# Kernel optimization log

Hardware: AMD Instinct MI355X
Metric: run time of the kernel (lower is better)

The kernel has to match this reference:

```python
import jax, jax.numpy as jnp
import numpy as np


def _conv1x1(x, w, b):
    # x: [B,C,H,W], w: [O,C], b: [O] -> [B,O,H,W]
    return jnp.einsum('bchw,oc->bohw', x, w) + b[None, :, None, None]


def setup_inputs() -> dict:
    key = jax.random.key(0)
    ks = jax.random.split(key, 11)
    B, C, Ci, H, W = 4, 256, 128, 64, 64
    s_in = 1.0 / np.sqrt(C)
    s_ci = 1.0 / np.sqrt(Ci)
    return {
        'x': jax.random.normal(ks[0], (B, C, H, W), jnp.float32),
        'g_w': jax.random.normal(ks[1], (Ci, C), jnp.float32) * s_in,
        'g_b': jax.random.normal(ks[2], (Ci,), jnp.float32) * 0.01,
        'theta_w': jax.random.normal(ks[3], (Ci, C), jnp.float32) * s_in,
        'theta_b': jax.random.normal(ks[4], (Ci,), jnp.float32) * 0.01,
        'phi_w': jax.random.normal(ks[5], (Ci, C), jnp.float32) * s_in,
        'phi_b': jax.random.normal(ks[6], (Ci,), jnp.float32) * 0.01,
        'wz_w': jax.random.normal(ks[7], (C, Ci), jnp.float32) * s_ci,
        'wz_b': jax.random.normal(ks[8], (C,), jnp.float32) * 0.01,
        'bn_gamma': jax.random.uniform(ks[9], (C,), jnp.float32, 0.5, 1.5),
        'bn_beta': jax.random.normal(ks[10], (C,), jnp.float32) * 0.01,
    }


def reference(x, g_w, g_b, theta_w, theta_b, phi_w, phi_b, wz_w, wz_b, bn_gamma, bn_beta):
    B, C, H, W = x.shape
    Ci = g_w.shape[0]
    N = H * W
    # 1x1 conv projections, flattened over spatial positions
    g_x = _conv1x1(x, g_w, g_b).reshape(B, Ci, N).transpose(0, 2, 1)       # [B,N,Ci]
    theta_x = _conv1x1(x, theta_w, theta_b).reshape(B, Ci, N)              # [B,Ci,N]
    phi_x = _conv1x1(x, phi_w, phi_b).reshape(B, Ci, N)                    # [B,Ci,N]
    # f[b, i, j] = theta_i . phi_j  -> [B,N,N]
    f = jnp.einsum('bci,bcj->bij', theta_x, phi_x)
    # NOTE: softmax over dim=1 (query axis) — faithful to original (non-standard)
    f_div_C = jax.nn.softmax(f, axis=1)
    y = jnp.einsum('bij,bjc->bic', f_div_C, g_x)                           # [B,N,Ci]
    y = y.transpose(0, 2, 1).reshape(B, Ci, H, W)                          # [B,Ci,H,W]
    # W_z: 1x1 conv + BatchNorm2d (training-mode batch statistics)
    w_y = _conv1x1(y, wz_w, wz_b)                                          # [B,C,H,W]
    mean = jnp.mean(w_y, axis=(0, 2, 3), keepdims=True)
    var = jnp.var(w_y, axis=(0, 2, 3), keepdims=True)
    w_y = (w_y - mean) * jax.lax.rsqrt(var + 1e-5)
    w_y = w_y * bn_gamma[None, :, None, None] + bn_beta[None, :, None, None]
    return w_y + x
```

## Files before the change

kernel.cpp:

```cpp
#include <hip/hip_runtime.h>


#define B_  4
#define C_  256
#define CI  128
#define N_  4096
#define NB  (B_*N_)
#define ISPLIT 16
#define MB_ (1u<<20)

typedef _Float16 f16;
typedef f16   f16x8 __attribute__((ext_vector_type(8)));
typedef f16   f16x4 __attribute__((ext_vector_type(4)));
typedef float f32x4 __attribute__((ext_vector_type(4)));

#define MFMA(a,b,c) __builtin_amdgcn_mfma_f32_16x16x32_f16(a,b,c,0,0,0)

#define GLD16(g, lp) __builtin_amdgcn_global_load_lds( \
    (const __attribute__((address_space(1))) void*)(g), \
    (__attribute__((address_space(3))) void*)(lp), 16, 0, 0)

#define OFF_THETA  0
#define OFF_PHI    (4u*MB_)
#define OFF_G      (8u*MB_)
#define OFF_YP     (12u*MB_)
#define OFF_WY     0
#define OFF_MD     (28u*MB_)
#define OFF_PS     (OFF_MD + 65536)
#define OFF_PSUM   (OFF_PS + ISPLIT*NB*4)
#define OFF_SSUM   (OFF_PSUM + 524288)
#define OFF_SSQ    (OFF_SSUM + 1024)
#define OFF_WCVT   (OFF_SSQ + 1024)
#define PSZ ((size_t)B_*N_*CI)

__global__ void k_init(const float* gw, const float* tw, const float* pw,
                       const float* zw, f16* wcvt) {
    int i = blockIdx.x * 256 + threadIdx.x;
    const float* s;
    int which = i >> 15;
    if (which == 0) s = gw; else if (which == 1) s = tw;
    else if (which == 2) s = pw; else s = zw;
    wcvt[i] = (f16)s[i & 32767];
}

__global__ __launch_bounds__(256) void k_proj(
        const float* __restrict__ x, const f16* __restrict__ wcvt,
        const float* __restrict__ gb, const float* __restrict__ tb,
        const float* __restrict__ pb,
        f16* __restrict__ thetaT, f16* __restrict__ phiT, f16* __restrict__ gC) {
    __shared__ __align__(16) f16 xT[32 * 264];
    int bb = blockIdx.x >> 7;
    int n0 = (blockIdx.x & 127) * 32;
    int t = threadIdx.x;

    const float* xb = x + (size_t)bb * C_ * N_;
    for (int rep = 0; rep < 8; rep++) {
        int lin = rep * 256 + t;
        int c = lin >> 3, np = (lin & 7) * 4;
        float4 v = *reinterpret_cast<const float4*>(xb + c * N_ + n0 + np);
        xT[(np + 0) * 264 + c] = (f16)v.x;
        xT[(np + 1) * 264 + c] = (f16)v.y;
        xT[(np + 2) * 264 + c] = (f16)v.z;
        xT[(np + 3) * 264 + c] = (f16)v.w;
    }
    __syncthreads();

    int w = t >> 6, l16 = t & 15, q = (t & 63) >> 4;
    int ci0 = w * 32;
    for (int proj = 0; proj < 3; proj++) {
        const f16* W0 = wcvt + proj * 32768;
        f32x4 acc[2][2] = {};
        for (int kk = 0; kk < 8; kk++) {
            f16x8 a0 = *reinterpret_cast<const f16x8*>(W0 + (ci0 + l16) * 256 + kk * 32 + q * 8);
            f16x8 a1 = *reinterpret_cast<const f16x8*>(W0 + (ci0 + 16 + l16) * 256 + kk * 32 + q * 8);
#pragma unroll
            for (int nt = 0; nt < 2; nt++) {
                f16x8 bv = *reinterpret_cast<const f16x8*>(&xT[(nt * 16 + l16) * 264 + kk * 32 + q * 8]);
                acc[0][nt] = MFMA(a0, bv, acc[0][nt]);
                acc[1][nt] = MFMA(a1, bv, acc[1][nt]);
            }
        }
        const float* bias = (proj == 0) ? gb : (proj == 1) ? tb : pb;
#pragma unroll
        for (int a = 0; a < 2; a++) {
#pragma unroll
            for (int nt = 0; nt < 2; nt++) {
                int n = n0 + nt * 16 + l16;
                int cib = ci0 + a * 16 + q * 4;
                if (proj == 0) {
#pragma unroll
                    for (int r = 0; r < 4; r++)
                        gC[((size_t)bb * CI + cib + r) * N_ + n] = (f16)(acc[a][nt][r] + bias[cib + r]);
                } else {
                    f16x4 v4;
#pragma unroll
                    for (int r = 0; r < 4; r++) v4[r] = (f16)(acc[a][nt][r] + bias[cib + r]);
                    f16* dst = (proj == 1 ? thetaT : phiT) + ((size_t)bb * N_ + n) * CI + cib;
                    *reinterpret_cast<f16x4*>(dst) = v4;
                }
            }
        }
    }
}

__global__ __launch_bounds__(256, 2) void k_cols(
        const f16* __restrict__ thetaT, const f16* __restrict__ phiT,
        float* __restrict__ ps) {
    __shared__ __align__(16) f16 thS[2][64 * 128];
    int id = blockIdx.x;
    int isp = id & 15, jb = (id >> 4) & 15, bb = id >> 8;
    int t = threadIdx.x, w = t >> 6, l = t & 63, l16 = t & 15, q = (t & 63) >> 4;
    int jw0 = jb * 256 + w * 64;

    f16x8 pf[4][4];
    const f16* pb = phiT + ((size_t)bb * N_ + jw0) * CI;
#pragma unroll
    for (int jt = 0; jt < 4; jt++)
#pragma unroll
        for (int kk = 0; kk < 4; kk++)
            pf[jt][kk] = *reinterpret_cast<const f16x8*>(pb + (jt * 16 + l16) * CI + kk * 32 + q * 8);

    const f16* thB = thetaT + ((size_t)bb * N_ + isp * 256) * CI;
    auto stage = [&](int bf, int it0) {
#pragma unroll
        for (int r = 0; r < 4; r++) {
            int p = r * 256 + w * 64 + l;
            int pi = p >> 4, pu = (p & 15) ^ (pi & 15);
            const char* ga = (const char*)(thB + (size_t)(it0 + pi) * CI) + pu * 16;
            GLD16(ga, &thS[bf][(r * 256 + w * 64) * 8]);
        }
    };

    float s[4] = {0.f, 0.f, 0.f, 0.f};
    stage(0, 0);
    __syncthreads();
    for (int it = 0; it < 4; it++) {
        int bf = it & 1;
        if (it + 1 < 4) stage(bf ^ 1, (it + 1) * 64);
#pragma unroll
        for (int ic = 0; ic < 4; ic++) {
            f16x8 av[4];
#pragma unroll
            for (int kk = 0; kk < 4; kk++)
                av[kk] = *reinterpret_cast<const f16x8*>(
                    &thS[bf][(ic * 16 + l16) * 128 + (((kk * 4 + q) ^ l16) * 8)]);
            f32x4 f[4] = {};
#pragma unroll
            for (int kk = 0; kk < 4; kk++)
#pragma unroll
                for (int jt = 0; jt < 4; jt++)
                    f[jt] = MFMA(av[kk], pf[jt][kk], f[jt]);
#pragma unroll
            for (int jt = 0; jt < 4; jt++)
                s[jt] += __expf(f[jt][0]) + __expf(f[jt][1])
                       + __expf(f[jt][2]) + __expf(f[jt][3]);
        }
        __syncthreads();
    }
#pragma unroll
    for (int jt = 0; jt < 4; jt++) {
        s[jt] += __shfl_xor(s[jt], 16);
        s[jt] += __shfl_xor(s[jt], 32);
    }
    if (q == 0) {
#pragma unroll
        for (int jt = 0; jt < 4; jt++)
            ps[isp * NB + bb * N_ + jw0 + jt * 16 + l16] = s[jt];
    }
}

__global__ void k_colmerge(const float* __restrict__ ps, float* __restrict__ md) {
    int j = blockIdx.x * 256 + threadIdx.x;
    float s = 0.f;
    for (int isp = 0; isp < ISPLIT; isp++) s += ps[isp * NB + j];
    md[j] = __logf(s);
}

__global__ __launch_bounds__(256, 2) void k_attn(
        const f16* __restrict__ thetaT, const f16* __restrict__ phiT,
        const f16* __restrict__ gC, const float* __restrict__ md,
        f16* __restrict__ yP) {
    __shared__ __align__(16) char smem[74752];
    f16 (*phiS)[64 * 128] = (f16(*)[64 * 128])smem;
    f16 (*gS)[128 * 64]   = (f16(*)[128 * 64])(smem + 32768);
    f16* Wl  = (f16*)(smem + 65536);
    f16* yTr = (f16*)smem;

    int jq = blockIdx.x & 3;
    int ib = blockIdx.x >> 2;
    int bb = ib >> 5;
    int i0 = (ib & 31) * 128;
    int t = threadIdx.x, w = t >> 6, l = t & 63, l16 = t & 15, q = (t & 63) >> 4;
    int jbase = jq * 1024;

    f16x8 ta[2][4];
    const f16* tb = thetaT + ((size_t)bb * N_ + i0 + w * 32 + l16) * CI;
#pragma unroll
    for (int s = 0; s < 2; s++)
#pragma unroll
        for (int kk = 0; kk < 4; kk++)
            ta[s][kk] = *reinterpret_cast<const f16x8*>(tb + s * 16 * CI + kk * 32 + q * 8);

    const f16* phiB = phiT + (size_t)bb * N_ * CI;
    const f16* gB   = gC   + (size_t)bb * CI * N_;
    const float* mdb = md + bb * N_;

    auto stage = [&](int bf, int j0g) {
#pragma unroll
        for (int r = 0; r < 4; r++) {
            int p = r * 256 + w * 64 + l;
            int ub = (r * 256 + w * 64) * 8;
            int pj = p >> 4, pu = (p & 15) ^ (pj & 15);
            const char* ga = (const char*)(phiB + (size_t)(j0g + pj) * CI) + pu * 16;
            GLD16(ga, &phiS[bf][ub]);
            int pc = p >> 3, pu2 = (p & 7) ^ (pc & 7);
            const char* ga2 = (const char*)(gB + (size_t)pc * N_ + j0g) + pu2 * 16;
            GLD16(ga2, &gS[bf][ub]);
        }
    };

    f32x4 yacc[2][8] = {};
    f16* Wlw = Wl + w * (32 * 36);
    stage(0, jbase);
    __syncthreads();
    for (int jt = 0; jt < 16; jt++) {
        int bf = jt & 1;
        if (jt + 1 < 16) stage(bf ^ 1, jbase + (jt + 1) * 64);
#pragma unroll
        for (int jh = 0; jh < 2; jh++) {
#pragma unroll
            for (int js2 = 0; js2 < 2; js2++) {
                int js = jh * 2 + js2;
                f32x4 f0 = {0,0,0,0}, f1 = {0,0,0,0};
#pragma unroll
                for (int kk = 0; kk < 4; kk++) {
                    f16x8 pv = *reinterpret_cast<const f16x8*>(
                        &phiS[bf][(js * 16 + l16) * 128 + (((kk * 4 + q) ^ l16) * 8)]);
                    f0 = MFMA(ta[0][kk], pv, f0);
                    f1 = MFMA(ta[1][kk], pv, f1);
                }
                float mdv = mdb[jbase + jt * 64 + js * 16 + l16];
#pragma unroll
                for (int r = 0; r < 4; r++) {
                    Wlw[(q * 4 + r) * 36 + js2 * 16 + l16]      = (f16)__expf(f0[r] - mdv);
                    Wlw[(16 + q * 4 + r) * 36 + js2 * 16 + l16] = (f16)__expf(f1[r] - mdv);
                }
            }
            f16x8 wf0 = *reinterpret_cast<const f16x8*>(&Wlw[l16 * 36 + q * 8]);
            f16x8 wf1 = *reinterpret_cast<const f16x8*>(&Wlw[(16 + l16) * 36 + q * 8]);
#pragma unroll
            for (int d = 0; d < 8; d++) {
                f16x8 gv = *reinterpret_cast<const f16x8*>(
                    &gS[bf][(d * 16 + l16) * 64 + (((jh * 4 + q) ^ (l16 & 7)) * 8)]);
                yacc[0][d] = MFMA(wf0, gv, yacc[0][d]);
                yacc[1][d] = MFMA(wf1, gv, yacc[1][d]);
            }
        }
        __syncthreads();
    }
    f16* yw = yTr + w * (32 * 136);
#pragma unroll
    for (int s = 0; s < 2; s++)
#pragma unroll
        for (int d = 0; d < 8; d++)
#pragma unroll
            for (int r = 0; r < 4; r++)
                yw[(s * 16 + q * 4 + r) * 136 + d * 16 + l16] = (f16)yacc[s][d][r];
    f16* yo = yP + (size_t)jq * PSZ + ((size_t)bb * N_ + i0 + w * 32) * CI;
#pragma unroll
    for (int rr = 0; rr < 8; rr++) {
        int chunk = rr * 64 + l;
        int il = chunk >> 4, u = chunk & 15;
        *reinterpret_cast<f16x8*>(yo + il * CI + u * 8) =
            *reinterpret_cast<const f16x8*>(&yw[il * 136 + u * 8]);
    }
}

__global__ __launch_bounds__(256) void k_wz(
        const f16* __restrict__ wzc, const f16* __restrict__ yP,
        const float* __restrict__ zb, f16* __restrict__ wy,
        float* __restrict__ psum) {
    int id = blockIdx.x;
    int nb = id & 63, bb = id >> 6;
    int t = threadIdx.x, w = t >> 6, l16 = t & 15, q = (t & 63) >> 4;
    int o0 = w * 64, n0 = nb * 64;
    f32x4 acc[4][4] = {};
#pragma unroll
    for (int kk = 0; kk < 4; kk++) {
        f16x8 bv[4];
#pragma unroll
        for (int nt = 0; nt < 4; nt++) {
            size_t yi = ((size_t)bb * N_ + n0 + nt * 16 + l16) * CI + kk * 32 + q * 8;
            f16x8 b0 = *reinterpret_cast<const f16x8*>(yP + yi);
            f16x8 b1 = *reinterpret_cast<const f16x8*>(yP + PSZ + yi);
            f16x8 b2 = *reinterpret_cast<const f16x8*>(yP + 2 * PSZ + yi);
            f16x8 b3 = *reinterpret_cast<const f16x8*>(yP + 3 * PSZ + yi);
            bv[nt] = (b0 + b1) + (b2 + b3);
        }
#pragma unroll
        for (int os = 0; os < 4; os++) {
            f16x8 av = *reinterpret_cast<const f16x8*>(
                wzc + (o0 + os * 16 + l16) * CI + kk * 32 + q * 8);
#pragma unroll
            for (int nt = 0; nt < 4; nt++)
                acc[os][nt] = MFMA(av, bv[nt], acc[os][nt]);
        }
    }
#pragma unroll
    for (int os = 0; os < 4; os++)
#pragma unroll
    for (int r = 0; r < 4; r++) {
        int o = o0 + os * 16 + q * 4 + r;
        float bias = zb[o];
        float sr = 0.f, qr = 0.f;
#pragma unroll
        for (int nt = 0; nt < 4; nt++) {
            float v = acc[os][nt][r] + bias;
            wy[((size_t)bb * C_ + o) * N_ + n0 + nt * 16 + l16] = (f16)v;
            sr += v; qr += v * v;
        }
#pragma unroll
        for (int off = 1; off < 16; off <<= 1) {
            sr += __shfl_xor(sr, off);
            qr += __shfl_xor(qr, off);
        }
        if (l16 == 0) {
            psum[(o * 2 + 0) * 256 + id] = sr;
            psum[(o * 2 + 1) * 256 + id] = qr;
        }
    }
}

__global__ void k_red(const float* __restrict__ psum, float* __restrict__ ssum,
                      float* __restrict__ ssq) {
    int b = blockIdx.x;
    int o = threadIdx.x;
    const float* src = psum + (o * 2 + b) * 256;
    float s = 0.f;
    for (int k = 0; k < 64; k++) {
        float4 v = reinterpret_cast<const float4*>(src)[k];
        s += v.x + v.y + v.z + v.w;
    }
    (b == 0 ? ssum : ssq)[o] = s;
}

__global__ void k_final(const f16* __restrict__ wy, const float* __restrict__ x,
                        const float* __restrict__ ssum, const float* __restrict__ ssq,
                        const float* __restrict__ gamma, const float* __restrict__ beta,
                        float* __restrict__ out) {
    int p = blockIdx.x * 256 + threadIdx.x;
    int c = (p >> 9) & 255;
    const float inv = 1.0f / 16384.0f;
    float mean = ssum[c] * inv;
    float var = ssq[c] * inv - mean * mean;
    float s = gamma[c] * rsqrtf(var + 1e-5f);
    float h = beta[c] - mean * s;
    f16x8 wv = reinterpret_cast<const f16x8*>(wy)[p];
    float4 x0 = reinterpret_cast<const float4*>(x)[2 * p];
    float4 x1 = reinterpret_cast<const float4*>(x)[2 * p + 1];
    float4 o0, o1;
    o0.x = (float)wv[0] * s + h + x0.x;
    o0.y = (float)wv[1] * s + h + x0.y;
    o0.z = (float)wv[2] * s + h + x0.z;
    o0.w = (float)wv[3] * s + h + x0.w;
    o1.x = (float)wv[4] * s + h + x1.x;
    o1.y = (float)wv[5] * s + h + x1.y;
    o1.z = (float)wv[6] * s + h + x1.z;
    o1.w = (float)wv[7] * s + h + x1.w;
    reinterpret_cast<float4*>(out)[2 * p] = o0;
    reinterpret_cast<float4*>(out)[2 * p + 1] = o1;
}

extern "C" void kernel_launch(void* const* d_in, const int* in_sizes, int n_in,
                              void* d_out, int out_size, void* d_ws, size_t ws_size,
                              hipStream_t stream) {
    const float* x     = (const float*)d_in[0];
    const float* gw    = (const float*)d_in[1];
    const float* gb    = (const float*)d_in[2];
    const float* tw    = (const float*)d_in[3];
    const float* tbv   = (const float*)d_in[4];
    const float* pw    = (const float*)d_in[5];
    const float* pb    = (const float*)d_in[6];
    const float* zw    = (const float*)d_in[7];
    const float* zb    = (const float*)d_in[8];
    const float* gamma = (const float*)d_in[9];
    const float* beta  = (const float*)d_in[10];

    char* ws = (char*)d_ws;
    f16* thetaT = (f16*)(ws + OFF_THETA);
    f16* phiT   = (f16*)(ws + OFF_PHI);
    f16* gC     = (f16*)(ws + OFF_G);
    f16* yP     = (f16*)(ws + OFF_YP);
    f16* wy     = (f16*)(ws + OFF_WY);
    f16* wcvt   = (f16*)(ws + OFF_WCVT);
    float* md   = (float*)(ws + OFF_MD);
    float* ps   = (float*)(ws + OFF_PS);
    float* psum = (float*)(ws + OFF_PSUM);
    float* ssum = (float*)(ws + OFF_SSUM);
    float* ssq  = (float*)(ws + OFF_SSQ);

    k_init<<<512, 256, 0, stream>>>(gw, tw, pw, zw, wcvt);
    k_proj<<<512, 256, 0, stream>>>(x, wcvt, gb, tbv, pb, thetaT, phiT, gC);
    k_cols<<<1024, 256, 0, stream>>>(thetaT, phiT, ps);
    k_colmerge<<<64, 256, 0, stream>>>(ps, md);
    k_attn<<<512, 256, 0, stream>>>(thetaT, phiT, gC, md, yP);
    k_wz<<<256, 256, 0, stream>>>(wcvt + 3 * 32768, yP, zb, wy, psum);
    k_red<<<2, 256, 0, stream>>>(psum, ssum, ssq);
    k_final<<<2048, 256, 0, stream>>>(wy, x, ssum, ssq, gamma, beta, (float*)d_out);
}
```

Before: 213.5 us.

## Switch attention kernel to 32x32x16 MFMA with in-register softmax weights via permlane swap

Rewrites the attention inner loop to use 32x32x16 MFMA tiles instead of 16x16x32. The S=phi^T theta product is computed transposed so that the exponentiated weights can be packed and rearranged in registers with permlane32_swap. This removes the per-wave LDS staging buffer for the weights, along with its writes, reads and the extra shared memory. The column-max values are now loaded as float4 vectors. The cost is more accumulator registers and a more intricate lane mapping, which could hurt occupancy or correctness.

```diff
diff --git a/kernel.cpp b/kernel.cpp
--- a/kernel.cpp
+++ b/kernel.cpp
@@ -13,8 +13,12 @@
 typedef f16   f16x8 __attribute__((ext_vector_type(8)));
 typedef f16   f16x4 __attribute__((ext_vector_type(4)));
 typedef float f32x4 __attribute__((ext_vector_type(4)));
-
-#define MFMA(a,b,c) __builtin_amdgcn_mfma_f32_16x16x32_f16(a,b,c,0,0,0)
+typedef float f32x16 __attribute__((ext_vector_type(16)));
+typedef unsigned u32x2 __attribute__((ext_vector_type(2)));
+typedef unsigned u32x4v __attribute__((ext_vector_type(4)));
+
+#define MFMA(a,b,c)   __builtin_amdgcn_mfma_f32_16x16x32_f16(a,b,c,0,0,0)
+#define MFMA32(a,b,c) __builtin_amdgcn_mfma_f32_32x32x16_f16(a,b,c,0,0,0)
 
 #define GLD16(g, lp) __builtin_amdgcn_global_load_lds( \
     (const __attribute__((address_space(1))) void*)(g), \
@@ -180,26 +184,24 @@
         const f16* __restrict__ thetaT, const f16* __restrict__ phiT,
         const f16* __restrict__ gC, const float* __restrict__ md,
         f16* __restrict__ yP) {
-    __shared__ __align__(16) char smem[74752];
+    __shared__ __align__(16) char smem[65536];
     f16 (*phiS)[64 * 128] = (f16(*)[64 * 128])smem;
     f16 (*gS)[128 * 64]   = (f16(*)[128 * 64])(smem + 32768);
-    f16* Wl  = (f16*)(smem + 65536);
     f16* yTr = (f16*)smem;
 
     int jq = blockIdx.x & 3;
     int ib = blockIdx.x >> 2;
     int bb = ib >> 5;
     int i0 = (ib & 31) * 128;
-    int t = threadIdx.x, w = t >> 6, l = t & 63, l16 = t & 15, q = (t & 63) >> 4;
+    int t = threadIdx.x, w = t >> 6, l = t & 63;
+    int l31 = l & 31, hi = l >> 5;
     int jbase = jq * 1024;
 
-    f16x8 ta[2][4];
-    const f16* tb = thetaT + ((size_t)bb * N_ + i0 + w * 32 + l16) * CI;
-#pragma unroll
-    for (int s = 0; s < 2; s++)
-#pragma unroll
-        for (int kk = 0; kk < 4; kk++)
-            ta[s][kk] = *reinterpret_cast<const f16x8*>(tb + s * 16 * CI + kk * 32 + q * 8);
+    f16x8 ta[8];
+    const f16* tb = thetaT + ((size_t)bb * N_ + i0 + w * 32 + l31) * CI + hi * 8;
+#pragma unroll
+    for (int kk = 0; kk < 8; kk++)
+        ta[kk] = *reinterpret_cast<const f16x8*>(tb + kk * 16);
 
     const f16* phiB = phiT + (size_t)bb * N_ * CI;
     const f16* gB   = gC   + (size_t)bb * CI * N_;
@@ -219,53 +221,73 @@
         }
     };
 
-    f32x4 yacc[2][8] = {};
-    f16* Wlw = Wl + w * (32 * 36);
+    f32x16 yacc[4] = {};
     stage(0, jbase);
     __syncthreads();
     for (int jt = 0; jt < 16; jt++) {
         int bf = jt & 1;
         if (jt + 1 < 16) stage(bf ^ 1, jbase + (jt + 1) * 64);
-#pragma unroll
-        for (int jh = 0; jh < 2; jh++) {
-#pragma unroll
-            for (int js2 = 0; js2 < 2; js2++) {
-                int js = jh * 2 + js2;
-                f32x4 f0 = {0,0,0,0}, f1 = {0,0,0,0};
-#pragma unroll
-                for (int kk = 0; kk < 4; kk++) {
-                    f16x8 pv = *reinterpret_cast<const f16x8*>(
-                        &phiS[bf][(js * 16 + l16) * 128 + (((kk * 4 + q) ^ l16) * 8)]);
-                    f0 = MFMA(ta[0][kk], pv, f0);
-                    f1 = MFMA(ta[1][kk], pv, f1);
-                }
-                float mdv = mdb[jbase + jt * 64 + js * 16 + l16];
-#pragma unroll
-                for (int r = 0; r < 4; r++) {
-                    Wlw[(q * 4 + r) * 36 + js2 * 16 + l16]      = (f16)__expf(f0[r] - mdv);
-                    Wlw[(16 + q * 4 + r) * 36 + js2 * 16 + l16] = (f16)__expf(f1[r] - mdv);
+
+        float mdv[2][16];
+#pragma unroll
+        for (int js = 0; js < 2; js++)
+#pragma unroll
+            for (int c = 0; c < 4; c++) {
+                float4 v = *reinterpret_cast<const float4*>(
+                    mdb + jbase + jt * 64 + js * 32 + c * 8 + hi * 4);
+                mdv[js][c * 4 + 0] = v.x; mdv[js][c * 4 + 1] = v.y;
+                mdv[js][c * 4 + 2] = v.z; mdv[js][c * 4 + 3] = v.w;
+            }
+
+        f32x16 facc[2] = {};
+#pragma unroll
+        for (int kk = 0; kk < 8; kk++) {
+#pragma unroll
+            for (int js = 0; js < 2; js++) {
+                f16x8 pv = *reinterpret_cast<const f16x8*>(
+                    &phiS[bf][(js * 32 + l31) * 128 + (((kk * 2 + hi) ^ (l31 & 15)) * 8)]);
+                facc[js] = MFMA32(pv, ta[kk], facc[js]);
+            }
+        }
+
+#pragma unroll
+        for (int js = 0; js < 2; js++) {
+#pragma unroll
+            for (int ch = 0; ch < 2; ch++) {
+                float e0 = __expf(facc[js][ch * 8 + 0] - mdv[js][ch * 8 + 0]);
+                float e1 = __expf(facc[js][ch * 8 + 1] - mdv[js][ch * 8 + 1]);
+                float e2 = __expf(facc[js][ch * 8 + 2] - mdv[js][ch * 8 + 2]);
+                float e3 = __expf(facc[js][ch * 8 + 3] - mdv[js][ch * 8 + 3]);
+                float e4 = __expf(facc[js][ch * 8 + 4] - mdv[js][ch * 8 + 4]);
+                float e5 = __expf(facc[js][ch * 8 + 5] - mdv[js][ch * 8 + 5]);
+                float e6 = __expf(facc[js][ch * 8 + 6] - mdv[js][ch * 8 + 6]);
+                float e7 = __expf(facc[js][ch * 8 + 7] - mdv[js][ch * 8 + 7]);
+                unsigned p01 = __builtin_bit_cast(unsigned, __builtin_amdgcn_cvt_pkrtz(e0, e1));
+                unsigned p23 = __builtin_bit_cast(unsigned, __builtin_amdgcn_cvt_pkrtz(e2, e3));
+                unsigned p45 = __builtin_bit_cast(unsigned, __builtin_amdgcn_cvt_pkrtz(e4, e5));
+                unsigned p67 = __builtin_bit_cast(unsigned, __builtin_amdgcn_cvt_pkrtz(e6, e7));
+                u32x2 s0 = __builtin_amdgcn_permlane32_swap(p01, p45, false, false);
+                u32x2 s1 = __builtin_amdgcn_permlane32_swap(p23, p67, false, false);
+                u32x4v wu = {s0[0], s1[0], s0[1], s1[1]};
+                f16x8 wfr = __builtin_bit_cast(f16x8, wu);
+                int jc = js * 2 + ch;
+#pragma unroll
+                for (int cs = 0; cs < 4; cs++) {
+                    f16x8 gv = *reinterpret_cast<const f16x8*>(
+                        &gS[bf][(cs * 32 + l31) * 64 + (((jc * 2 + hi) ^ (l31 & 7)) * 8)]);
+                    yacc[cs] = MFMA32(wfr, gv, yacc[cs]);
                 }
             }
-            f16x8 wf0 = *reinterpret_cast<const f16x8*>(&Wlw[l16 * 36 + q * 8]);
-            f16x8 wf1 = *reinterpret_cast<const f16x8*>(&Wlw[(16 + l16) * 36 + q * 8]);
-#pragma unroll
-            for (int d = 0; d < 8; d++) {
-                f16x8 gv = *reinterpret_cast<const f16x8*>(
-                    &gS[bf][(d * 16 + l16) * 64 + (((jh * 4 + q) ^ (l16 & 7)) * 8)]);
-                yacc[0][d] = MFMA(wf0, gv, yacc[0][d]);
-                yacc[1][d] = MFMA(wf1, gv, yacc[1][d]);
-            }
         }
         __syncthreads();
     }
+
     f16* yw = yTr + w * (32 * 136);
 #pragma unroll
-    for (int s = 0; s < 2; s++)
-#pragma unroll
-        for (int d = 0; d < 8; d++)
-#pragma unroll
-            for (int r = 0; r < 4; r++)
-                yw[(s * 16 + q * 4 + r) * 136 + d * 16 + l16] = (f16)yacc[s][d][r];
+    for (int cs = 0; cs < 4; cs++)
+#pragma unroll
+        for (int r = 0; r < 16; r++)
+            yw[((r & 3) + 8 * (r >> 2) + 4 * hi) * 136 + cs * 32 + l31] = (f16)yacc[cs][r];
     f16* yo = yP + (size_t)jq * PSZ + ((size_t)bb * N_ + i0 + w * 32) * CI;
 #pragma unroll
     for (int rr = 0; rr < 8; rr++) {
```

Result: faster. 202.8 us (-5.0%).
